# Kernel optimization log

Hardware: AMD Instinct MI355X
Metric: run time of the kernel (lower is better)

The kernel has to match this reference:

```python
import jax, jax.numpy as jnp
import numpy as np

N_NODES = 50000
N_EDGES = 800000
D = 128
BATCHSIZE = 64


def setup_inputs() -> dict:
    key = jax.random.key(0)
    k1, k2, k3, k4 = jax.random.split(key, 4)
    x = jax.random.normal(k1, (N_NODES, D), dtype=jnp.float32)
    eps = jnp.zeros((1,), dtype=jnp.float32)
    W_pred = jax.random.normal(k2, (D, D), dtype=jnp.float32) * (1.0 / np.sqrt(D))
    b_pred = jnp.zeros((D,), dtype=jnp.float32)
    edge_index = jax.random.randint(k3, (2, N_EDGES), 0, N_NODES, dtype=jnp.int64)
    batch = jnp.sort(jax.random.randint(k4, (N_NODES,), 0, BATCHSIZE, dtype=jnp.int64))
    return {"x": x, "eps": eps, "W_pred": W_pred, "b_pred": b_pred,
            "edge_index": edge_index, "batch": batch}


def reference(x, eps, W_pred, b_pred, edge_index, batch):
    src, dst = edge_index[0], edge_index[1]
    # spmm: sum of neighbor features for each destination node [N, D]
    agg = jax.ops.segment_sum(x[src], dst, num_segments=N_NODES)
    # eps-weighted self update (apply_func=None, norm=None)
    out = (1.0 + eps) * x + agg
    out = jax.nn.relu(out)  # activation='relu'
    # linear_prediction then per-graph scatter-add pooling
    pooled = out @ W_pred + b_pred  # [N, pooled_features]
    pooled2 = jax.ops.segment_sum(pooled, batch, num_segments=BATCHSIZE)  # [B, pooled]
    return out, pooled2
```

## Files before the change

### kernel.cpp

```cpp
#include <hip/hip_runtime.h>
#include <hip/hip_bf16.h>

#define N_NODES 50000
#define N_EDGES 800000
#define D 128
#define BATCHSIZE 64

#define CHUNK_BITS 7
#define CHUNK 128
#define NBUCKETS 391
#define NBUCKETS_PAD 392
#define CAP 2400

#define FB_TILE 4096
#define NTILES ((N_EDGES + FB_TILE - 1) / FB_TILE)
#define SLICES 4
#define SLICE_B 98
#define FB_THREADS 256
#define FB_GRID (NTILES * SLICES)

#define GCHUNK 64
#define GT 512
#define GGRID (NBUCKETS * 2)

__device__ inline unsigned short f2bf(float f) {
    union { float f; unsigned u; } c; c.f = f;
    unsigned u = c.u;
    return (unsigned short)((u + 0x7fffu + ((u >> 16) & 1u)) >> 16);
}

__device__ inline float4 bf4_to_f4(uint2 u) {
    union { unsigned u; float f; } a, b, c, d;
    a.u = u.x << 16; b.u = u.x & 0xffff0000u;
    c.u = u.y << 16; d.u = u.y & 0xffff0000u;
    float4 r; r.x = a.f; r.y = b.f; r.z = c.f; r.w = d.f;
    return r;
}

__global__ __launch_bounds__(FB_THREADS) void bin_convert_kernel(
    const float* __restrict__ x,
    unsigned short* __restrict__ xb,
    const int* __restrict__ edge_index,
    int* __restrict__ gcur,
    int* __restrict__ bucket,
    float* __restrict__ pooled2)
{
    __shared__ int hist[SLICE_B];
    __shared__ int gbase[SLICE_B];

    int t = threadIdx.x;
    int blk = blockIdx.x;

    for (int i = blk * FB_THREADS + t; i < BATCHSIZE * D; i += FB_GRID * FB_THREADS)
        pooled2[i] = 0.0f;

    if (xb != nullptr) {
        const int TOT4 = N_NODES * D / 4;
        for (int i = blk * FB_THREADS + t; i < TOT4; i += FB_GRID * FB_THREADS) {
            float4 v = *(const float4*)(x + (size_t)i * 4);
            uint2 pk;
            pk.x = (unsigned)f2bf(v.x) | ((unsigned)f2bf(v.y) << 16);
            pk.y = (unsigned)f2bf(v.z) | ((unsigned)f2bf(v.w) << 16);
            *(uint2*)(xb + (size_t)i * 4) = pk;
        }
    }

    int tile = blk >> 2;
    int sl   = blk & 3;
    int blo  = sl * SLICE_B;
    int bhi  = blo + SLICE_B; if (bhi > NBUCKETS) bhi = NBUCKETS;
    int nb   = bhi - blo;

    for (int i = t; i < SLICE_B; i += FB_THREADS) hist[i] = 0;
    __syncthreads();

    int base = tile * FB_TILE;
    int lim = N_EDGES - base; if (lim > FB_TILE) lim = FB_TILE;

    int bkt[16];
    int pack[16];
#pragma unroll
    for (int j = 0; j < 4; ++j) {
        int rel = j * FB_THREADS + t;
        int e4 = rel * 4;
#pragma unroll
        for (int k = 0; k < 4; ++k) bkt[j * 4 + k] = -1;
        if (e4 < lim) {
            int4 s4 = *(const int4*)(edge_index + base + e4);
            int4 d4 = *(const int4*)(edge_index + N_EDGES + base + e4);
            int ss[4] = { s4.x, s4.y, s4.z, s4.w };
            int dd[4] = { d4.x, d4.y, d4.z, d4.w };
#pragma unroll
            for (int k = 0; k < 4; ++k) {
                int b = (dd[k] >> CHUNK_BITS) - blo;
                if ((unsigned)b < (unsigned)nb) {
                    bkt[j * 4 + k] = b;
                    pack[j * 4 + k] = (ss[k] << CHUNK_BITS) | (dd[k] & (CHUNK - 1));
                    atomicAdd(&hist[b], 1);
                }
            }
        }
    }
    __syncthreads();

    for (int i = t; i < nb; i += FB_THREADS) {
        int c = hist[i];
        gbase[i] = c ? atomicAdd(&gcur[blo + i], c) : 0;
        hist[i] = 0;
    }
    __syncthreads();

#pragma unroll
    for (int k = 0; k < 16; ++k) {
        int b = bkt[k];
        if (b >= 0) {
            int pos = gbase[b] + atomicAdd(&hist[b], 1);
            if (pos < CAP) bucket[(size_t)(blo + b) * CAP + pos] = pack[k];
        }
    }
}

template<bool BF16>
__global__ __launch_bounds__(GT, 8) void gather_kernel(
    const float* __restrict__ x,
    const unsigned short* __restrict__ xb,
    const float* __restrict__ eps,
    const int* __restrict__ batch,
    const int* __restrict__ gcur,
    const int* __restrict__ bucket,
    const float* __restrict__ W,
    const float* __restrict__ b_pred,
    float* __restrict__ out,
    float* __restrict__ pooled2)
{
    __shared__ int   sorted[CAP];
    __shared__ int   hist[GCHUNK];
    __shared__ int   offs[GCHUNK + 1];
    __shared__ int   cursor[GCHUNK];
    __shared__ float pool[8 * D];
    __shared__ int   pcount[8];

    int blk = blockIdx.x;
    int c = blk >> 1;
    int h = blk & 1;
    int t = threadIdx.x;
    int lane = t & 31;
    int g = t >> 5;

    if (t < GCHUNK) hist[t] = 0;
    if (t < 8) pcount[t] = 0;
    for (int i = t; i < 8 * D; i += GT) pool[i] = 0.0f;
    int cnt = gcur[c];
    if (cnt > CAP) cnt = CAP;
    __syncthreads();

    const int hbase = h << 6;
    const int* brow = bucket + (size_t)c * CAP;

    for (int i = t; i < cnt; i += GT) {
        int p = brow[i];
        int dloc = (p & (CHUNK - 1)) - hbase;
        if ((unsigned)dloc < (unsigned)GCHUNK) atomicAdd(&hist[dloc], 1);
    }
    __syncthreads();

    if (t < GCHUNK) {
        int tot = hist[t];
        int incl = tot;
#pragma unroll
        for (int o = 1; o < 64; o <<= 1) {
            int y = __shfl_up(incl, o, 64);
            if (t >= o) incl += y;
        }
        offs[t] = incl - tot;
        cursor[t] = incl - tot;
        if (t == GCHUNK - 1) offs[GCHUNK] = incl;
    }
    __syncthreads();

    for (int i = t; i < cnt; i += GT) {
        int p = brow[i];
        int dloc = (p & (CHUNK - 1)) - hbase;
        if ((unsigned)dloc < (unsigned)GCHUNK) {
            int pos = atomicAdd(&cursor[dloc], 1);
            sorted[pos] = p >> CHUNK_BITS;
        }
    }
    __syncthreads();

    int node0 = (c << CHUNK_BITS) + hbase;
    int bnode = node0 < N_NODES ? node0 : N_NODES - 1;
    int base_b = batch[bnode];
    float scale = 1.0f + eps[0];
    int dv_cur = -1;
    float4 ps = make_float4(0.f, 0.f, 0.f, 0.f);

#pragma unroll
    for (int k = 0; k < 4; ++k) {
        int dloc = 4 * g + k;
        int node = node0 + dloc;
        if (node >= N_NODES) break;
        int start = offs[dloc], end = offs[dloc + 1];
        float4 acc = make_float4(0.f, 0.f, 0.f, 0.f);
        int i = start;
        if (BF16) {
            for (; i + 8 <= end; i += 8) {
                int s0 = sorted[i],     s1 = sorted[i + 1];
                int s2 = sorted[i + 2], s3 = sorted[i + 3];
                int s4 = sorted[i + 4], s5 = sorted[i + 5];
                int s6 = sorted[i + 6], s7 = sorted[i + 7];
                uint2 u0 = *(const uint2*)(xb + (size_t)s0 * D + lane * 4);
                uint2 u1 = *(const uint2*)(xb + (size_t)s1 * D + lane * 4);
                uint2 u2 = *(const uint2*)(xb + (size_t)s2 * D + lane * 4);
                uint2 u3 = *(const uint2*)(xb + (size_t)s3 * D + lane * 4);
                uint2 u4 = *(const uint2*)(xb + (size_t)s4 * D + lane * 4);
                uint2 u5 = *(const uint2*)(xb + (size_t)s5 * D + lane * 4);
                uint2 u6 = *(const uint2*)(xb + (size_t)s6 * D + lane * 4);
                uint2 u7 = *(const uint2*)(xb + (size_t)s7 * D + lane * 4);
                float4 v0 = bf4_to_f4(u0), v1 = bf4_to_f4(u1);
                float4 v2 = bf4_to_f4(u2), v3 = bf4_to_f4(u3);
                float4 v4 = bf4_to_f4(u4), v5 = bf4_to_f4(u5);
                float4 v6 = bf4_to_f4(u6), v7 = bf4_to_f4(u7);
                acc.x += ((v0.x + v1.x) + (v2.x + v3.x)) + ((v4.x + v5.x) + (v6.x + v7.x));
                acc.y += ((v0.y + v1.y) + (v2.y + v3.y)) + ((v4.y + v5.y) + (v6.y + v7.y));
                acc.z += ((v0.z + v1.z) + (v2.z + v3.z)) + ((v4.z + v5.z) + (v6.z + v7.z));
                acc.w += ((v0.w + v1.w) + (v2.w + v3.w)) + ((v4.w + v5.w) + (v6.w + v7.w));
            }
            for (; i < end; ++i) {
                uint2 u0 = *(const uint2*)(xb + (size_t)sorted[i] * D + lane * 4);
                float4 v0 = bf4_to_f4(u0);
                acc.x += v0.x; acc.y += v0.y; acc.z += v0.z; acc.w += v0.w;
            }
        } else {
            for (; i + 4 <= end; i += 4) {
                int s0 = sorted[i], s1 = sorted[i + 1];
                int s2 = sorted[i + 2], s3 = sorted[i + 3];
                const float4 v0 = *(const float4*)(x + (size_t)s0 * D + lane * 4);
                const float4 v1 = *(const float4*)(x + (size_t)s1 * D + lane * 4);
                const float4 v2 = *(const float4*)(x + (size_t)s2 * D + lane * 4);
                const float4 v3 = *(const float4*)(x + (size_t)s3 * D + lane * 4);
                acc.x += (v0.x + v1.x) + (v2.x + v3.x);
                acc.y += (v0.y + v1.y) + (v2.y + v3.y);
                acc.z += (v0.z + v1.z) + (v2.z + v3.z);
                acc.w += (v0.w + v1.w) + (v2.w + v3.w);
            }
            for (; i < end; ++i) {
                const float4 v0 = *(const float4*)(x + (size_t)sorted[i] * D + lane * 4);
                acc.x += v0.x; acc.y += v0.y; acc.z += v0.z; acc.w += v0.w;
            }
        }
        const float4 xv = *(const float4*)(x + (size_t)node * D + lane * 4);
        float4 o;
        o.x = fmaxf(fmaf(scale, xv.x, acc.x), 0.0f);
        o.y = fmaxf(fmaf(scale, xv.y, acc.y), 0.0f);
        o.z = fmaxf(fmaf(scale, xv.z, acc.z), 0.0f);
        o.w = fmaxf(fmaf(scale, xv.w, acc.w), 0.0f);
        *(float4*)(out + (size_t)node * D + lane * 4) = o;

        int dv = batch[node] - base_b;
        if (dv < 8) {
            if (dv != dv_cur) {
                if (dv_cur >= 0) {
                    float* pp = &pool[dv_cur * D + lane * 4];
                    atomicAdd(pp + 0, ps.x); atomicAdd(pp + 1, ps.y);
                    atomicAdd(pp + 2, ps.z); atomicAdd(pp + 3, ps.w);
                }
                ps = make_float4(0.f, 0.f, 0.f, 0.f);
                dv_cur = dv;
            }
            ps.x += o.x; ps.y += o.y; ps.z += o.z; ps.w += o.w;
            if (lane == 0) atomicAdd(&pcount[dv], 1);
        }
    }
    if (dv_cur >= 0) {
        float* pp = &pool[dv_cur * D + lane * 4];
        atomicAdd(pp + 0, ps.x); atomicAdd(pp + 1, ps.y);
        atomicAdd(pp + 2, ps.z); atomicAdd(pp + 3, ps.w);
    }
    __syncthreads();

    int lastnode = node0 + GCHUNK - 1;
    if (lastnode >= N_NODES) lastnode = N_NODES - 1;
    int used = batch[lastnode] - base_b + 1;
    if (used > 8) used = 8;
    if (used < 0) used = 0;
    if (t < D) {
        for (int dv = 0; dv < used; ++dv) {
            float acc = (float)pcount[dv] * b_pred[t];
            const float* prow = &pool[dv * D];
#pragma unroll 8
            for (int k = 0; k < D; ++k) {
                acc = fmaf(prow[k], W[(size_t)k * D + t], acc);
            }
            atomicAdd(&pooled2[(size_t)(base_b + dv) * D + t], acc);
        }
    }
}


__global__ void edge_scatter_kernel(const float* __restrict__ x,
                                    const int* __restrict__ edge_index,
                                    float* __restrict__ agg) {
    int tid = blockIdx.x * blockDim.x + threadIdx.x;
    int lane = tid & 31;
    int e = tid >> 5;
    if (e >= N_EDGES) return;
    int src = edge_index[e];
    int dst = edge_index[N_EDGES + e];
    const float4 v = *(const float4*)(x + (size_t)src * D + lane * 4);
    float* dp = agg + (size_t)dst * D + lane * 4;
    atomicAdd(dp + 0, v.x);
    atomicAdd(dp + 1, v.y);
    atomicAdd(dp + 2, v.z);
    atomicAdd(dp + 3, v.w);
}

__global__ void finalize_kernel(const float* __restrict__ x,
                                const float* __restrict__ eps,
                                const int* __restrict__ batch,
                                float* __restrict__ out,
                                float* __restrict__ Sf,
                                float* __restrict__ counts) {
    int tid = blockIdx.x * blockDim.x + threadIdx.x;
    int lane = tid & 31;
    int node = tid >> 5;
    if (node >= N_NODES) return;
    float scale = 1.0f + eps[0];
    const float4 xv = *(const float4*)(x + (size_t)node * D + lane * 4);
    float4 av = *(float4*)(out + (size_t)node * D + lane * 4);
    float4 o;
    o.x = fmaxf(fmaf(scale, xv.x, av.x), 0.0f);
    o.y = fmaxf(fmaf(scale, xv.y, av.y), 0.0f);
    o.z = fmaxf(fmaf(scale, xv.z, av.z), 0.0f);
    o.w = fmaxf(fmaf(scale, xv.w, av.w), 0.0f);
    *(float4*)(out + (size_t)node * D + lane * 4) = o;
    int b = batch[node];
    float* sp = Sf + (size_t)b * D + lane * 4;
    atomicAdd(sp + 0, o.x);
    atomicAdd(sp + 1, o.y);
    atomicAdd(sp + 2, o.z);
    atomicAdd(sp + 3, o.w);
    if (lane == 0) atomicAdd(counts + b, 1.0f);
}

__global__ void pool_gemm_fallback_kernel(const float* __restrict__ Sf,
                                          const float* __restrict__ counts,
                                          const float* __restrict__ W,
                                          const float* __restrict__ b_pred,
                                          float* __restrict__ pooled2) {
    int b = blockIdx.x;
    int j = threadIdx.x;
    float acc = counts[b] * b_pred[j];
    const float* srow = Sf + (size_t)b * D;
#pragma unroll 8
    for (int k = 0; k < D; ++k) {
        acc = fmaf(srow[k], W[(size_t)k * D + j], acc);
    }
    pooled2[(size_t)b * D + j] = acc;
}

extern "C" void kernel_launch(void* const* d_in, const int* in_sizes, int n_in,
                              void* d_out, int out_size, void* d_ws, size_t ws_size,
                              hipStream_t stream) {
    const float* x      = (const float*)d_in[0];
    const float* eps    = (const float*)d_in[1];
    const float* W_pred = (const float*)d_in[2];
    const float* b_pred = (const float*)d_in[3];
    const int*   eidx   = (const int*)d_in[4];
    const int*   batch  = (const int*)d_in[5];

    float* out     = (float*)d_out;
    float* pooled2 = (float*)d_out + (size_t)N_NODES * D;

    const size_t base_ints = (size_t)NBUCKETS_PAD + (size_t)NBUCKETS * CAP;
    const size_t need_mid  = base_ints * 4;
    const size_t need_full = (base_ints + (size_t)N_NODES * D / 2) * 4;

    if (ws_size >= need_mid) {
        int* gcur   = (int*)d_ws;
        int* bucket = (int*)d_ws + NBUCKETS_PAD;
        bool full = (ws_size >= need_full);
        unsigned short* xb = full ? (unsigned short*)((int*)d_ws + base_ints) : nullptr;

        hipMemsetAsync(gcur, 0, (size_t)NBUCKETS_PAD * 4, stream);

        bin_convert_kernel<<<FB_GRID, FB_THREADS, 0, stream>>>(
            x, xb, eidx, gcur, bucket, pooled2);
        if (full) {
            gather_kernel<true><<<GGRID, GT, 0, stream>>>(
                x, xb, eps, batch, gcur, bucket, W_pred, b_pred, out, pooled2);
        } else {
            gather_kernel<false><<<GGRID, GT, 0, stream>>>(
                x, (const unsigned short*)nullptr, eps, batch, gcur, bucket,
                W_pred, b_pred, out, pooled2);
        }
    } else {
        float* Sf      = (float*)d_ws;
        float* countsf = (float*)d_ws + BATCHSIZE * D;
        hipMemsetAsync(out, 0, (size_t)N_NODES * D * sizeof(float), stream);
        hipMemsetAsync(d_ws, 0, (BATCHSIZE * D + BATCHSIZE) * sizeof(float), stream);
        {
            long long total = (long long)N_EDGES * 32;
            int blocks = (int)((total + 255) / 256);
            edge_scatter_kernel<<<blocks, 256, 0, stream>>>(x, eidx, out);
        }
        {
            long long total = (long long)N_NODES * 32;
            int blocks = (int)((total + 255) / 256);
            finalize_kernel<<<blocks, 256, 0, stream>>>(x, eps, batch, out, Sf, countsf);
        }
        pool_gemm_fallback_kernel<<<BATCHSIZE, D, 0, stream>>>(Sf, countsf, W_pred, b_pred, pooled2);
    }
}
```

Measured before the change: 155.3 us.

## Widen bf16 gather loads to 16B with half-warp edge split; drop bucket slicing

The gather kernel's bf16 path now has each half-warp fetch a different neighbour row with 16-byte loads (8 bf16 per lane). The two half sums are combined with a cross-lane shuffle, and the output/pool feature offsets are remapped to match. The binning kernel drops its 4-way bucket slicing, so each block reads its edge tile only once and histograms all buckets in shared memory, using smaller tiles. The bf16 conversion also writes 16-byte packs. The aim is fewer, wider memory transactions and no repeated edge reads, at the cost of extra shuffles and a lower occupancy hint (6 instead of 8 blocks).

```diff
diff --git a/kernel.cpp b/kernel.cpp
--- a/kernel.cpp
+++ b/kernel.cpp
@@ -12,29 +12,20 @@
 #define NBUCKETS_PAD 392
 #define CAP 2400
 
-#define FB_TILE 4096
+#define FB_TILE 2048
 #define NTILES ((N_EDGES + FB_TILE - 1) / FB_TILE)
-#define SLICES 4
-#define SLICE_B 98
 #define FB_THREADS 256
-#define FB_GRID (NTILES * SLICES)
+#define FB_GRID NTILES
+#define EPT 8
 
 #define GCHUNK 64
 #define GT 512
 #define GGRID (NBUCKETS * 2)
 
-__device__ inline unsigned short f2bf(float f) {
+__device__ inline unsigned f2bf(float f) {
     union { float f; unsigned u; } c; c.f = f;
     unsigned u = c.u;
-    return (unsigned short)((u + 0x7fffu + ((u >> 16) & 1u)) >> 16);
-}
-
-__device__ inline float4 bf4_to_f4(uint2 u) {
-    union { unsigned u; float f; } a, b, c, d;
-    a.u = u.x << 16; b.u = u.x & 0xffff0000u;
-    c.u = u.y << 16; d.u = u.y & 0xffff0000u;
-    float4 r; r.x = a.f; r.y = b.f; r.z = c.f; r.w = d.f;
-    return r;
+    return (u + 0x7fffu + ((u >> 16) & 1u)) >> 16;
 }
 
 __global__ __launch_bounds__(FB_THREADS) void bin_convert_kernel(
@@ -45,8 +36,8 @@
     int* __restrict__ bucket,
     float* __restrict__ pooled2)
 {
-    __shared__ int hist[SLICE_B];
-    __shared__ int gbase[SLICE_B];
+    __shared__ int hist[NBUCKETS_PAD];
+    __shared__ int gbase[NBUCKETS_PAD];
 
     int t = threadIdx.x;
     int blk = blockIdx.x;
@@ -55,34 +46,30 @@
         pooled2[i] = 0.0f;
 
     if (xb != nullptr) {
-        const int TOT4 = N_NODES * D / 4;
-        for (int i = blk * FB_THREADS + t; i < TOT4; i += FB_GRID * FB_THREADS) {
-            float4 v = *(const float4*)(x + (size_t)i * 4);
-            uint2 pk;
-            pk.x = (unsigned)f2bf(v.x) | ((unsigned)f2bf(v.y) << 16);
-            pk.y = (unsigned)f2bf(v.z) | ((unsigned)f2bf(v.w) << 16);
-            *(uint2*)(xb + (size_t)i * 4) = pk;
-        }
-    }
-
-    int tile = blk >> 2;
-    int sl   = blk & 3;
-    int blo  = sl * SLICE_B;
-    int bhi  = blo + SLICE_B; if (bhi > NBUCKETS) bhi = NBUCKETS;
-    int nb   = bhi - blo;
-
-    for (int i = t; i < SLICE_B; i += FB_THREADS) hist[i] = 0;
-    __syncthreads();
-
-    int base = tile * FB_TILE;
+        const int TOT8 = N_NODES * D / 8;
+        for (int i = blk * FB_THREADS + t; i < TOT8; i += FB_GRID * FB_THREADS) {
+            float4 v0 = *(const float4*)(x + (size_t)i * 8);
+            float4 v1 = *(const float4*)(x + (size_t)i * 8 + 4);
+            uint4 pk;
+            pk.x = f2bf(v0.x) | (f2bf(v0.y) << 16);
+            pk.y = f2bf(v0.z) | (f2bf(v0.w) << 16);
+            pk.z = f2bf(v1.x) | (f2bf(v1.y) << 16);
+            pk.w = f2bf(v1.z) | (f2bf(v1.w) << 16);
+            *(uint4*)(xb + (size_t)i * 8) = pk;
+        }
+    }
+
+    for (int i = t; i < NBUCKETS_PAD; i += FB_THREADS) hist[i] = 0;
+    __syncthreads();
+
+    int base = blk * FB_TILE;
     int lim = N_EDGES - base; if (lim > FB_TILE) lim = FB_TILE;
 
-    int bkt[16];
-    int pack[16];
-#pragma unroll
-    for (int j = 0; j < 4; ++j) {
-        int rel = j * FB_THREADS + t;
-        int e4 = rel * 4;
+    int bkt[EPT];
+    int pack[EPT];
+#pragma unroll
+    for (int j = 0; j < EPT / 4; ++j) {
+        int e4 = (j * FB_THREADS + t) * 4;
 #pragma unroll
         for (int k = 0; k < 4; ++k) bkt[j * 4 + k] = -1;
         if (e4 < lim) {
@@ -92,36 +79,42 @@
             int dd[4] = { d4.x, d4.y, d4.z, d4.w };
 #pragma unroll
             for (int k = 0; k < 4; ++k) {
-                int b = (dd[k] >> CHUNK_BITS) - blo;
-                if ((unsigned)b < (unsigned)nb) {
-                    bkt[j * 4 + k] = b;
-                    pack[j * 4 + k] = (ss[k] << CHUNK_BITS) | (dd[k] & (CHUNK - 1));
-                    atomicAdd(&hist[b], 1);
-                }
-            }
-        }
-    }
-    __syncthreads();
-
-    for (int i = t; i < nb; i += FB_THREADS) {
+                int b = dd[k] >> CHUNK_BITS;
+                bkt[j * 4 + k] = b;
+                pack[j * 4 + k] = (ss[k] << CHUNK_BITS) | (dd[k] & (CHUNK - 1));
+                atomicAdd(&hist[b], 1);
+            }
+        }
+    }
+    __syncthreads();
+
+    for (int i = t; i < NBUCKETS; i += FB_THREADS) {
         int c = hist[i];
-        gbase[i] = c ? atomicAdd(&gcur[blo + i], c) : 0;
+        gbase[i] = c ? atomicAdd(&gcur[i], c) : 0;
         hist[i] = 0;
     }
     __syncthreads();
 
 #pragma unroll
-    for (int k = 0; k < 16; ++k) {
+    for (int k = 0; k < EPT; ++k) {
         int b = bkt[k];
         if (b >= 0) {
             int pos = gbase[b] + atomicAdd(&hist[b], 1);
-            if (pos < CAP) bucket[(size_t)(blo + b) * CAP + pos] = pack[k];
-        }
-    }
-}
+            if (pos < CAP) bucket[(size_t)b * CAP + pos] = pack[k];
+        }
+    }
+}
+
+#define ACC8(u) do {                                                     \
+    union { unsigned q; float f; } lo_, hi_;                             \
+    lo_.q = (u).x << 16; hi_.q = (u).x & 0xffff0000u; a0 += lo_.f; a1 += hi_.f; \
+    lo_.q = (u).y << 16; hi_.q = (u).y & 0xffff0000u; a2 += lo_.f; a3 += hi_.f; \
+    lo_.q = (u).z << 16; hi_.q = (u).z & 0xffff0000u; a4 += lo_.f; a5 += hi_.f; \
+    lo_.q = (u).w << 16; hi_.q = (u).w & 0xffff0000u; a6 += lo_.f; a7 += hi_.f; \
+} while (0)
 
 template<bool BF16>
-__global__ __launch_bounds__(GT, 8) void gather_kernel(
+__global__ __launch_bounds__(GT, 6) void gather_kernel(
     const float* __restrict__ x,
     const unsigned short* __restrict__ xb,
     const float* __restrict__ eps,
@@ -146,6 +139,8 @@
     int t = threadIdx.x;
     int lane = t & 31;
     int g = t >> 5;
+    int sub = lane >> 4;
+    int li  = lane & 15;
 
     if (t < GCHUNK) hist[t] = 0;
     if (t < 8) pcount[t] = 0;
@@ -195,43 +190,54 @@
     int dv_cur = -1;
     float4 ps = make_float4(0.f, 0.f, 0.f, 0.f);
 
+    const int fo = BF16 ? (li * 8 + sub * 4) : (lane * 4);
+
 #pragma unroll
     for (int k = 0; k < 4; ++k) {
         int dloc = 4 * g + k;
         int node = node0 + dloc;
         if (node >= N_NODES) break;
         int start = offs[dloc], end = offs[dloc + 1];
-        float4 acc = make_float4(0.f, 0.f, 0.f, 0.f);
-        int i = start;
+        float4 acc;
         if (BF16) {
-            for (; i + 8 <= end; i += 8) {
-                int s0 = sorted[i],     s1 = sorted[i + 1];
-                int s2 = sorted[i + 2], s3 = sorted[i + 3];
-                int s4 = sorted[i + 4], s5 = sorted[i + 5];
-                int s6 = sorted[i + 6], s7 = sorted[i + 7];
-                uint2 u0 = *(const uint2*)(xb + (size_t)s0 * D + lane * 4);
-                uint2 u1 = *(const uint2*)(xb + (size_t)s1 * D + lane * 4);
-                uint2 u2 = *(const uint2*)(xb + (size_t)s2 * D + lane * 4);
-                uint2 u3 = *(const uint2*)(xb + (size_t)s3 * D + lane * 4);
-                uint2 u4 = *(const uint2*)(xb + (size_t)s4 * D + lane * 4);
-                uint2 u5 = *(const uint2*)(xb + (size_t)s5 * D + lane * 4);
-                uint2 u6 = *(const uint2*)(xb + (size_t)s6 * D + lane * 4);
-                uint2 u7 = *(const uint2*)(xb + (size_t)s7 * D + lane * 4);
-                float4 v0 = bf4_to_f4(u0), v1 = bf4_to_f4(u1);
-                float4 v2 = bf4_to_f4(u2), v3 = bf4_to_f4(u3);
-                float4 v4 = bf4_to_f4(u4), v5 = bf4_to_f4(u5);
-                float4 v6 = bf4_to_f4(u6), v7 = bf4_to_f4(u7);
-                acc.x += ((v0.x + v1.x) + (v2.x + v3.x)) + ((v4.x + v5.x) + (v6.x + v7.x));
-                acc.y += ((v0.y + v1.y) + (v2.y + v3.y)) + ((v4.y + v5.y) + (v6.y + v7.y));
-                acc.z += ((v0.z + v1.z) + (v2.z + v3.z)) + ((v4.z + v5.z) + (v6.z + v7.z));
-                acc.w += ((v0.w + v1.w) + (v2.w + v3.w)) + ((v4.w + v5.w) + (v6.w + v7.w));
-            }
-            for (; i < end; ++i) {
-                uint2 u0 = *(const uint2*)(xb + (size_t)sorted[i] * D + lane * 4);
-                float4 v0 = bf4_to_f4(u0);
-                acc.x += v0.x; acc.y += v0.y; acc.z += v0.z; acc.w += v0.w;
-            }
+            float a0 = 0.f, a1 = 0.f, a2 = 0.f, a3 = 0.f;
+            float a4 = 0.f, a5 = 0.f, a6 = 0.f, a7 = 0.f;
+            int i = start;
+            for (; i + 16 <= end; i += 16) {
+                int e0 = sorted[i + 0  + sub];
+                int e1 = sorted[i + 2  + sub];
+                int e2 = sorted[i + 4  + sub];
+                int e3 = sorted[i + 6  + sub];
+                int e4 = sorted[i + 8  + sub];
+                int e5 = sorted[i + 10 + sub];
+                int e6 = sorted[i + 12 + sub];
+                int e7 = sorted[i + 14 + sub];
+                uint4 u0 = *(const uint4*)(xb + (size_t)e0 * D + li * 8);
+                uint4 u1 = *(const uint4*)(xb + (size_t)e1 * D + li * 8);
+                uint4 u2 = *(const uint4*)(xb + (size_t)e2 * D + li * 8);
+                uint4 u3 = *(const uint4*)(xb + (size_t)e3 * D + li * 8);
+                uint4 u4 = *(const uint4*)(xb + (size_t)e4 * D + li * 8);
+                uint4 u5 = *(const uint4*)(xb + (size_t)e5 * D + li * 8);
+                uint4 u6 = *(const uint4*)(xb + (size_t)e6 * D + li * 8);
+                uint4 u7 = *(const uint4*)(xb + (size_t)e7 * D + li * 8);
+                ACC8(u0); ACC8(u1); ACC8(u2); ACC8(u3);
+                ACC8(u4); ACC8(u5); ACC8(u6); ACC8(u7);
+            }
+            for (; i < end; i += 2) {
+                int e = i + sub;
+                if (e < end) {
+                    uint4 u = *(const uint4*)(xb + (size_t)sorted[e] * D + li * 8);
+                    ACC8(u);
+                }
+            }
+            a0 += __shfl_xor(a0, 16); a1 += __shfl_xor(a1, 16);
+            a2 += __shfl_xor(a2, 16); a3 += __shfl_xor(a3, 16);
+            a4 += __shfl_xor(a4, 16); a5 += __shfl_xor(a5, 16);
+            a6 += __shfl_xor(a6, 16); a7 += __shfl_xor(a7, 16);
+            acc = sub ? make_float4(a4, a5, a6, a7) : make_float4(a0, a1, a2, a3);
         } else {
+            acc = make_float4(0.f, 0.f, 0.f, 0.f);
+            int i = start;
             for (; i + 4 <= end; i += 4) {
                 int s0 = sorted[i], s1 = sorted[i + 1];
                 int s2 = sorted[i + 2], s3 = sorted[i + 3];
@@ -249,19 +255,20 @@
                 acc.x += v0.x; acc.y += v0.y; acc.z += v0.z; acc.w += v0.w;
             }
         }
-        const float4 xv = *(const float4*)(x + (size_t)node * D + lane * 4);
+
+        const float4 xv = *(const float4*)(x + (size_t)node * D + fo);
         float4 o;
         o.x = fmaxf(fmaf(scale, xv.x, acc.x), 0.0f);
         o.y = fmaxf(fmaf(scale, xv.y, acc.y), 0.0f);
         o.z = fmaxf(fmaf(scale, xv.z, acc.z), 0.0f);
         o.w = fmaxf(fmaf(scale, xv.w, acc.w), 0.0f);
-        *(float4*)(out + (size_t)node * D + lane * 4) = o;
+        *(float4*)(out + (size_t)node * D + fo) = o;
 
         int dv = batch[node] - base_b;
         if (dv < 8) {
             if (dv != dv_cur) {
                 if (dv_cur >= 0) {
-                    float* pp = &pool[dv_cur * D + lane * 4];
+                    float* pp = &pool[dv_cur * D + fo];
                     atomicAdd(pp + 0, ps.x); atomicAdd(pp + 1, ps.y);
                     atomicAdd(pp + 2, ps.z); atomicAdd(pp + 3, ps.w);
                 }
@@ -273,7 +280,7 @@
         }
     }
     if (dv_cur >= 0) {
-        float* pp = &pool[dv_cur * D + lane * 4];
+        float* pp = &pool[dv_cur * D + fo];
         atomicAdd(pp + 0, ps.x); atomicAdd(pp + 1, ps.y);
         atomicAdd(pp + 2, ps.z); atomicAdd(pp + 3, ps.w);
     }
```

Result: slower. 183.0 us (+17.8%).
